# Kernel optimization log

Hardware: AMD Instinct MI355X
Metric: run time of the kernel (lower is better)

Reference implementation:

```python
import jax, jax.numpy as jnp
import numpy as np
from jax import lax

# ---- static graph layout: GPT-2-small-like full edge-pruning config ----
N_LAYERS, H = 12, 12
V_TOTAL = 2 + N_LAYERS * (H + 1)  # wte, wpe, then per layer: H attn outputs + 1 mlp

def _layer_dims(L):
    Vq = 2 + L * (H + 1)  # vertices visible to q/k/v at layer L (strictly upstream)
    Vm = Vq + H           # mlp additionally sees same-layer attn outputs
    return Vq, Vm

_LAYER_BASE = []
_p = 0
for _L in range(N_LAYERS):
    _LAYER_BASE.append(_p)
    _Vq, _Vm = _layer_dims(_L)
    _p += 3 * H * _Vq + _Vm  # q,k,v edges for all heads, then mlp edges
_LM_BASE = _p
P_TOTAL = _p + V_TOTAL       # lm_head reads every vertex


def _keep(Rch):
    """Given per-vertex reachability Rch (bz, V_TOTAL) bool, build the per-edge
    keep mask (bz, P_TOTAL): an edge survives iff its output vertex AND its
    input vertex are both reachable (== ~dangling in the torch code)."""
    bz = Rch.shape[0]
    parts = []
    for L in range(N_LAYERS):
        Vq, Vm = _layer_dims(L)
        a0 = 2 + L * (H + 1)
        ar = Rch[:, a0:a0 + H]        # (bz, H) attn_output-L-h reach
        mr = Rch[:, a0 + H]           # (bz,)  mlp-L reach
        kq = ar[:, None, :, None] & Rch[:, None, None, :Vq]  # (bz,3,H,Vq)
        parts.append(jnp.broadcast_to(kq, (bz, 3, H, Vq)).reshape(bz, 3 * H * Vq))
        parts.append(mr[:, None] & Rch[:, :Vm])
        del kq
    parts.append(Rch)                 # lm_head edges: keep iff input reachable
    return jnp.concatenate(parts, axis=1)


def _prune_dangling_edges(masks):
    bz = masks.shape[0]
    # --- forward reachability (reach-to-input), no-grad boolean sweep ---
    pos = masks > 0.0
    R = jnp.ones((bz, 2), bool)  # wte, wpe always reachable
    for L in range(N_LAYERS):
        Vq, Vm = _layer_dims(L)
        b = _LAYER_BASE[L]
        qkv = pos[:, b:b + 3 * H * Vq].reshape(bz, 3, H, Vq)
        # head reachable iff q AND k AND v each have >=1 live reachable input
        ar = jnp.all(jnp.any(qkv & R[:, None, None, :], axis=-1), axis=1)  # (bz,H)
        R = jnp.concatenate([R, ar], axis=1)                               # size Vm
        mm = pos[:, b + 3 * H * Vq: b + 3 * H * Vq + Vm]
        mr = jnp.any(mm & R, axis=-1)
        R = jnp.concatenate([R, mr[:, None]], axis=1)
    masks = jnp.where(_keep(R), masks, 0.0)
    # --- backward reachability (reach-to-output) on the pruned masks ---
    pos = masks > 0.0
    O = pos[:, _LM_BASE:]  # (bz, V_TOTAL): vertices fed into lm_head
    for L in range(N_LAYERS - 1, -1, -1):
        Vq, Vm = _layer_dims(L)
        b = _LAYER_BASE[L]
        a0 = 2 + L * (H + 1)
        # mlp first (it may make same-layer attn outputs output-reachable)
        mm = pos[:, b + 3 * H * Vq: b + 3 * H * Vq + Vm]
        O = O.at[:, :Vm].set(O[:, :Vm] | (mm & O[:, a0 + H][:, None]))
        qkv = pos[:, b:b + 3 * H * Vq].reshape(bz, 3, H, Vq)
        contrib = jnp.any(qkv & O[:, None, a0:a0 + H, None], axis=(1, 2))  # (bz,Vq)
        O = O.at[:, :Vq].set(O[:, :Vq] | contrib)
    masks = jnp.where(_keep(O), masks, 0.0)
    return masks


def setup_inputs() -> dict:
    key = jax.random.key(0)
    k1, k2 = jax.random.split(key)
    bz = 1024
    sample_params = jax.random.normal(k1, (P_TOTAL,), dtype=jnp.float32)
    unif = jax.random.uniform(k2, (bz, P_TOTAL), dtype=jnp.float32)
    return {"sample_params": sample_params, "unif": unif}


def reference(sample_params, unif):
    bz = unif.shape[0]
    prob = jnp.broadcast_to(jax.nn.sigmoid(sample_params)[None, :], unif.shape)
    window = lax.stop_gradient(prob * (1.0 - prob))  # detached window size
    prob = window * prob + (1.0 - window) * lax.stop_gradient(prob)
    masks = jnp.clip((prob - unif) / window + 0.5, 0.0, 1.0)
    masks = _prune_dangling_edges(masks)
    active = (masks > 0.001) & (masks < 1.0 - 0.001)
    n_samples = jnp.sum(active, axis=0).astype(masks.dtype)  # (P,)
    grad_wts = lax.stop_gradient(
        jnp.where(n_samples < 1.0, 0.0, bz / jnp.maximum(n_samples, 1.0)))
    masks = grad_wts * masks + (1.0 - grad_wts) * lax.stop_gradient(masks)
    return masks
```

## Files before the change

kernel.cpp:

```cpp
#include <hip/hip_runtime.h>
#include <stdint.h>

#define NL   12
#define PTOT 32936
#define LMB  32778
#define NCH  515
#define NCHP 520
#define NGRP 129
#define BMW  (NGRP * 4)
#define TPAD (NGRP * 256)
#define NSEG 445
#define TPB  512
#define NWV  (TPB / 64)
#define NITER ((NGRP + NWV - 1) / NWV)

typedef float vf4 __attribute__((ext_vector_type(4)));

__device__ __constant__ int c_base[NL] = {0,86,653,1701,3230,5240,7731,10703,14156,18090,22505,27401};

__device__ __forceinline__ uint64_t ext(const uint64_t* P, uint32_t off) {
  uint32_t w = off >> 6, s = off & 63;
  uint64_t lo = P[w], hi = P[w + 1];
  return s ? ((lo >> s) | (hi << (64 - s))) : lo;
}

__device__ __forceinline__ uint64_t rbit(uint64_t r0, uint64_t r1, uint64_t r2, uint32_t idx) {
  uint64_t w = idx < 64 ? r0 : (idx < 128 ? r1 : r2);
  return (w >> (idx & 63)) & 1ull;
}

__device__ __forceinline__ uint64_t rext(uint64_t a0, uint64_t a1, uint64_t a2, uint32_t off) {
  uint32_t w = off >> 6, s = off & 63;
  uint64_t lo = (w == 0) ? a0 : ((w == 1) ? a1 : ((w == 2) ? a2 : 0ull));
  uint64_t hi = (w == 0) ? a1 : ((w == 1) ? a2 : 0ull);
  return s ? ((lo >> s) | (hi << (64 - s))) : lo;
}

__device__ __forceinline__ void orAt(uint64_t& r0, uint64_t& r1, uint64_t& r2,
                                     uint64_t val, uint32_t pos) {
  uint32_t w = pos >> 6, s = pos & 63;
  uint64_t lo = val << s;
  uint64_t hi = s ? (val >> (64 - s)) : 0ull;
  if (w == 0) { r0 |= lo; r1 |= hi; }
  else if (w == 1) { r1 |= lo; r2 |= hi; }
  else { r2 |= lo; }
}

__device__ __forceinline__ void maskLen(uint32_t len, uint64_t& m0, uint64_t& m1, uint64_t& m2) {
  m0 = (len >= 64) ? ~0ull : ((1ull << len) - 1ull);
  m1 = (len <= 64) ? 0ull : ((len >= 128) ? ~0ull : ((1ull << (len - 64)) - 1ull));
  m2 = (len <= 128) ? 0ull : ((1ull << (len - 128)) - 1ull);
}

__device__ __forceinline__ uint32_t ext12(uint64_t O0, uint64_t O1, uint64_t O2, uint32_t pos) {
  uint32_t w = pos >> 6, s = pos & 63;
  uint64_t lo = (w == 0) ? O0 : ((w == 1) ? O1 : O2);
  uint64_t hi = (w == 0) ? O1 : ((w == 1) ? O2 : 0ull);
  uint64_t v = s ? ((lo >> s) | (hi << (64 - s))) : lo;
  return (uint32_t)v & 0xFFFu;
}

__device__ __forceinline__ uint64_t spread4(uint64_t x) {
  x = (x | (x << 24)) & 0x000000FF000000FFull;
  x = (x | (x << 12)) & 0x000F000F000F000Full;
  x = (x | (x << 6))  & 0x0303030303030303ull;
  x = (x | (x << 3))  & 0x1111111111111111ull;
  return x;
}

__global__ void init_tables(const float* __restrict__ sp, float* __restrict__ pr,
                            float* __restrict__ wd) {
  int p = blockIdx.x * blockDim.x + threadIdx.x;
  if (p >= TPAD) return;
  if (p < PTOT) {
    float x = sp[p];
    float s = 1.0f / (1.0f + expf(-x));
    float w = __fmul_rn(s, __fsub_rn(1.0f, s));
    float pv = __fadd_rn(__fmul_rn(w, s), __fmul_rn(__fsub_rn(1.0f, w), s));
    pr[p] = pv; wd[p] = w;
  } else {
    pr[p] = 0.0f; wd[p] = 1.0f;
  }
}

__global__ __launch_bounds__(TPB, 4) void fused_kernel(const float* __restrict__ unif,
                                                       const vf4* __restrict__ pr4,
                                                       const vf4* __restrict__ wd4,
                                                       float* __restrict__ out) {
  __shared__ uint64_t sPos[NCHP];
  __shared__ uint64_t sKeep[NCHP];
  __shared__ uint64_t sLv[4];

  const int tid  = threadIdx.x;
  const int lane = tid & 63;
  const int wv   = tid >> 6;
  const int row  = blockIdx.x;
  const vf4* up4 = (const vf4*)(unif + (size_t)row * PTOT);
  vf4*       op4 = (vf4*)(out + (size_t)row * PTOT);

  vf4 mv[NITER];

  {
    vf4 u = {0.f,0.f,0.f,0.f}, p = {0.f,0.f,0.f,0.f}, w = {1.f,1.f,1.f,1.f};
    {
      int e4 = wv * 64 + lane;
      u = up4[e4]; p = pr4[e4]; w = wd4[e4];
    }
#pragma unroll
    for (int k = 0; k < NITER; ++k) {
      const int G = wv + k * NWV;
      const bool act = G < NGRP;
      vf4 un = {0.f,0.f,0.f,0.f}, pn = {0.f,0.f,0.f,0.f}, wn = {1.f,1.f,1.f,1.f};
      if (k + 1 < NITER) {
        const int Gn = G + NWV;
        if (Gn < NGRP) {
          int e4n = Gn * 64 + lane;
          bool inbn = e4n < (PTOT / 4);
          un = inbn ? up4[e4n] : (vf4){0.f,0.f,0.f,0.f};
          pn = pr4[e4n]; wn = wd4[e4n];
        }
      }
      if (act) {
        int e4 = G * 64 + lane;
        bool inb = e4 < (PTOT / 4);
        float m0 = __fadd_rn(__fdiv_rn(__fsub_rn(p.x, u.x), w.x), 0.5f);
        float m1 = __fadd_rn(__fdiv_rn(__fsub_rn(p.y, u.y), w.y), 0.5f);
        float m2 = __fadd_rn(__fdiv_rn(__fsub_rn(p.z, u.z), w.z), 0.5f);
        float m3 = __fadd_rn(__fdiv_rn(__fsub_rn(p.w, u.w), w.w), 0.5f);
        mv[k] = (vf4){m0, m1, m2, m3};
        uint64_t b0 = __ballot(inb && (m0 > 0.0f));
        uint64_t b1 = __ballot(inb && (m1 > 0.0f));
        uint64_t b2 = __ballot(inb && (m2 > 0.0f));
        uint64_t b3 = __ballot(inb && (m3 > 0.0f));
        if (lane < 4) {
          uint64_t v = (lane == 0) ? b0 : (lane == 1) ? b1 : (lane == 2) ? b2 : b3;
          sKeep[G * 4 + lane] = v;
        }
      }
      u = un; p = pn; w = wn;
    }
  }
  __syncthreads();

  for (int G = tid; G < NGRP; G += TPB) {
    uint64_t b0 = sKeep[4 * G], b1 = sKeep[4 * G + 1];
    uint64_t b2 = sKeep[4 * G + 2], b3 = sKeep[4 * G + 3];
#pragma unroll
    for (int q = 0; q < 4; ++q) {
      uint64_t v = spread4((b0 >> (16 * q)) & 0xFFFFull)
                 | (spread4((b1 >> (16 * q)) & 0xFFFFull) << 1)
                 | (spread4((b2 >> (16 * q)) & 0xFFFFull) << 2)
                 | (spread4((b3 >> (16 * q)) & 0xFFFFull) << 3);
      sPos[4 * G + q] = v;
      sKeep[4 * G + q] = 0ull;
    }
  }
  for (int w = BMW + tid; w < NCHP; w += TPB) { sPos[w] = 0ull; sKeep[w] = 0ull; }
  __syncthreads();

  if (tid < 64) {
    uint64_t R0 = 3ull, R1 = 0ull, R2 = 0ull;
    const int g = lane;
#pragma unroll
    for (int L = 0; L < NL; ++L) {
      const int Vq = 2 + 13 * L;
      const int b  = c_base[L];
      bool pred = false;
      if (g < 36) {
        uint32_t off = (uint32_t)(b + g * Vq);
        uint64_t e0 = ext(sPos, off), e1 = ext(sPos, off + 64), e2 = ext(sPos, off + 128);
        pred = ((e0 & R0) | (e1 & R1) | (e2 & R2)) != 0ull;
      }
      uint64_t bal = __ballot(pred);
      uint64_t ar  = bal & (bal >> 12) & (bal >> 24) & 0xFFFull;
      orAt(R0, R1, R2, ar, (uint32_t)Vq);
      const int Vm = Vq + 12;
      uint32_t offm = (uint32_t)(b + 36 * Vq);
      uint64_t e0 = ext(sPos, offm), e1 = ext(sPos, offm + 64), e2 = ext(sPos, offm + 128);
      uint64_t mr = (((e0 & R0) | (e1 & R1) | (e2 & R2)) != 0ull) ? 1ull : 0ull;
      orAt(R0, R1, R2, mr, (uint32_t)Vm);
    }

    uint64_t O0 = ext(sPos, LMB)       & R0;
    uint64_t O1 = ext(sPos, LMB + 64)  & R1;
    uint64_t O2 = ext(sPos, LMB + 128) & ((1ull << 30) - 1ull) & R2;
    const int hg = g % 12;
#pragma unroll
    for (int L = NL - 1; L >= 0; --L) {
      const int Vq = 2 + 13 * L, Vm = Vq + 12;
      const int b  = c_base[L];
      if (rbit(O0, O1, O2, (uint32_t)Vm)) {
        uint64_t m0, m1, m2; maskLen((uint32_t)Vm, m0, m1, m2);
        uint32_t offm = (uint32_t)(b + 36 * Vq);
        O0 |= ext(sPos, offm)       & R0 & m0;
        O1 |= ext(sPos, offm + 64)  & R1 & m1;
        O2 |= ext(sPos, offm + 128) & R2 & m2;
      }
      uint32_t h12 = ext12(O0, O1, O2, (uint32_t)Vq);
      uint64_t q0, q1, q2; maskLen((uint32_t)Vq, q0, q1, q2);
      uint64_t c0 = 0ull, c1 = 0ull, c2 = 0ull;
      if (g < 36 && ((h12 >> hg) & 1u)) {
        uint32_t off = (uint32_t)(b + g * Vq);
        c0 = ext(sPos, off)       & R0 & q0;
        c1 = ext(sPos, off + 64)  & R1 & q1;
        c2 = ext(sPos, off + 128) & R2 & q2;
      }
#pragma unroll
      for (int d = 32; d; d >>= 1) {
        c0 |= __shfl_xor((unsigned long long)c0, d);
        c1 |= __shfl_xor((unsigned long long)c1, d);
        c2 |= __shfl_xor((unsigned long long)c2, d);
      }
      O0 |= c0; O1 |= c1; O2 |= c2;
    }
    if (lane == 0) {
      sLv[0] = R0 & O0; sLv[1] = R1 & O1; sLv[2] = R2 & O2; sLv[3] = 0ull;
    }
  }
  __syncthreads();

  {
    const uint64_t l0 = sLv[0], l1 = sLv[1], l2 = sLv[2];
    for (int s = tid; s < NSEG; s += TPB) {
      uint32_t p0, len;
      bool olive;
      if (s == NSEG - 1) {
        p0 = LMB; len = 158; olive = true;
      } else {
        int L = s / 37, j = s - L * 37;
        int Vq = 2 + 13 * L, b = c_base[L];
        if (j < 36) { p0 = (uint32_t)(b + j * Vq); len = (uint32_t)Vq;
                      olive = rbit(l0, l1, l2, (uint32_t)(Vq + (j % 12))) != 0ull; }
        else        { p0 = (uint32_t)(b + 36 * Vq); len = (uint32_t)(Vq + 12);
                      olive = rbit(l0, l1, l2, (uint32_t)(Vq + 12)) != 0ull; }
      }
      if (!olive) continue;
      uint32_t w0 = p0 >> 6, s0 = p0 & 63;
      uint64_t first = l0;
      if (len < 64) first &= (1ull << len) - 1ull;
      atomicOr((unsigned long long*)&sKeep[w0], (unsigned long long)(first << s0));
      uint32_t done = 64 - s0;
      uint32_t w = w0 + 1;
      while (done < len) {
        uint64_t v = rext(l0, l1, l2, done);
        uint32_t rem = len - done;
        if (rem < 64) v &= (1ull << rem) - 1ull;
        atomicOr((unsigned long long*)&sKeep[w], (unsigned long long)v);
        done += 64; ++w;
      }
    }
  }
  __syncthreads();

  {
    const int sh = 4 * (lane & 15);
    const int kw0 = lane >> 4;
#pragma unroll
    for (int k = 0; k < NITER; ++k) {
      const int G = wv + k * NWV;
      if (G >= NGRP) continue;
      int e4 = G * 64 + lane;
      bool inb = e4 < (PTOT / 4);
      uint32_t kb = (uint32_t)(sKeep[G * 4 + kw0] >> sh) & 0xFu;
      vf4 m = mv[k];
      if (inb) {
        vf4 o;
        o.x = (kb & 1u) ? fminf(fmaxf(m.x, 0.0f), 1.0f) : 0.0f;
        o.y = (kb & 2u) ? fminf(fmaxf(m.y, 0.0f), 1.0f) : 0.0f;
        o.z = (kb & 4u) ? fminf(fmaxf(m.z, 0.0f), 1.0f) : 0.0f;
        o.w = (kb & 8u) ? fminf(fmaxf(m.w, 0.0f), 1.0f) : 0.0f;
        __builtin_nontemporal_store(o, &op4[e4]);
      }
    }
  }
}

extern "C" void kernel_launch(void* const* d_in, const int* in_sizes, int n_in,
                              void* d_out, int out_size, void* d_ws, size_t ws_size,
                              hipStream_t stream) {
  const float* sp   = (const float*)d_in[0];
  const float* unif = (const float*)d_in[1];
  float* out = (float*)d_out;
  char* ws = (char*)d_ws;
  float* pr = (float*)ws;
  float* wd = (float*)(ws + 132096);
  int bz = in_sizes[1] / PTOT;

  init_tables<<<dim3(TPAD / 256), dim3(256), 0, stream>>>(sp, pr, wd);
  fused_kernel<<<dim3(bz), dim3(TPB), 0, stream>>>(
      unif, (const vf4*)pr, (const vf4*)wd, out);
}
```

Baseline: 252.3 us.

## Deepen load prefetch, pack positivity bits in-wave, drop extra sync pass

The load loop now prefetches unif four iterations ahead and prob/window two ahead instead of one. The spread4 bit-interleaving is done directly by lanes 0-3 after the ballots, removing a separate pass over shared memory and one __syncthreads. Clamping moves into the first phase, and launch bounds drop from 4 to 3 blocks per SM to give room for the extra in-flight registers. The aim is more memory-level parallelism and fewer barriers, at the cost of lower occupancy.

```diff
diff --git a/kernel.cpp b/kernel.cpp
--- a/kernel.cpp
+++ b/kernel.cpp
@@ -83,7 +83,7 @@
   }
 }
 
-__global__ __launch_bounds__(TPB, 4) void fused_kernel(const float* __restrict__ unif,
+__global__ __launch_bounds__(TPB, 3) void fused_kernel(const float* __restrict__ unif,
                                                        const vf4* __restrict__ pr4,
                                                        const vf4* __restrict__ wd4,
                                                        float* __restrict__ out) {
@@ -99,63 +99,50 @@
   vf4*       op4 = (vf4*)(out + (size_t)row * PTOT);
 
   vf4 mv[NITER];
-
-  {
-    vf4 u = {0.f,0.f,0.f,0.f}, p = {0.f,0.f,0.f,0.f}, w = {1.f,1.f,1.f,1.f};
-    {
-      int e4 = wv * 64 + lane;
-      u = up4[e4]; p = pr4[e4]; w = wd4[e4];
-    }
-#pragma unroll
-    for (int k = 0; k < NITER; ++k) {
-      const int G = wv + k * NWV;
-      const bool act = G < NGRP;
-      vf4 un = {0.f,0.f,0.f,0.f}, pn = {0.f,0.f,0.f,0.f}, wn = {1.f,1.f,1.f,1.f};
-      if (k + 1 < NITER) {
-        const int Gn = G + NWV;
-        if (Gn < NGRP) {
-          int e4n = Gn * 64 + lane;
-          bool inbn = e4n < (PTOT / 4);
-          un = inbn ? up4[e4n] : (vf4){0.f,0.f,0.f,0.f};
-          pn = pr4[e4n]; wn = wd4[e4n];
-        }
-      }
-      if (act) {
-        int e4 = G * 64 + lane;
-        bool inb = e4 < (PTOT / 4);
-        float m0 = __fadd_rn(__fdiv_rn(__fsub_rn(p.x, u.x), w.x), 0.5f);
-        float m1 = __fadd_rn(__fdiv_rn(__fsub_rn(p.y, u.y), w.y), 0.5f);
-        float m2 = __fadd_rn(__fdiv_rn(__fsub_rn(p.z, u.z), w.z), 0.5f);
-        float m3 = __fadd_rn(__fdiv_rn(__fsub_rn(p.w, u.w), w.w), 0.5f);
-        mv[k] = (vf4){m0, m1, m2, m3};
-        uint64_t b0 = __ballot(inb && (m0 > 0.0f));
-        uint64_t b1 = __ballot(inb && (m1 > 0.0f));
-        uint64_t b2 = __ballot(inb && (m2 > 0.0f));
-        uint64_t b3 = __ballot(inb && (m3 > 0.0f));
-        if (lane < 4) {
-          uint64_t v = (lane == 0) ? b0 : (lane == 1) ? b1 : (lane == 2) ? b2 : b3;
-          sKeep[G * 4 + lane] = v;
-        }
-      }
-      u = un; p = pn; w = wn;
-    }
-  }
-  __syncthreads();
-
-  for (int G = tid; G < NGRP; G += TPB) {
-    uint64_t b0 = sKeep[4 * G], b1 = sKeep[4 * G + 1];
-    uint64_t b2 = sKeep[4 * G + 2], b3 = sKeep[4 * G + 3];
-#pragma unroll
-    for (int q = 0; q < 4; ++q) {
-      uint64_t v = spread4((b0 >> (16 * q)) & 0xFFFFull)
-                 | (spread4((b1 >> (16 * q)) & 0xFFFFull) << 1)
-                 | (spread4((b2 >> (16 * q)) & 0xFFFFull) << 2)
-                 | (spread4((b3 >> (16 * q)) & 0xFFFFull) << 3);
-      sPos[4 * G + q] = v;
-      sKeep[4 * G + q] = 0ull;
-    }
-  }
-  for (int w = BMW + tid; w < NCHP; w += TPB) { sPos[w] = 0ull; sKeep[w] = 0ull; }
+  vf4 ub[4], pb[2], wb[2];
+
+#define LDU(K) do { int G_ = wv + (K) * NWV; if (G_ < NGRP) {                  \
+    int e4_ = G_ * 64 + lane;                                                  \
+    ub[(K) % 4] = (e4_ < (PTOT / 4)) ? up4[e4_] : (vf4){0.f,0.f,0.f,0.f}; } } while (0)
+#define LDPW(K) do { int G_ = wv + (K) * NWV; if (G_ < NGRP) {                 \
+    int e4_ = G_ * 64 + lane;                                                  \
+    pb[(K) % 2] = pr4[e4_]; wb[(K) % 2] = wd4[e4_]; } } while (0)
+
+  LDU(0); LDU(1); LDU(2); LDU(3); LDPW(0); LDPW(1);
+  for (int w = tid; w < NCHP; w += TPB) sKeep[w] = 0ull;
+  for (int w = BMW + tid; w < NCHP; w += TPB) sPos[w] = 0ull;
+
+#pragma unroll
+  for (int k = 0; k < NITER; ++k) {
+    const int G = wv + k * NWV;
+    if (G < NGRP) {
+      vf4 u = ub[k % 4], p = pb[k % 2], w = wb[k % 2];
+      int e4 = G * 64 + lane;
+      bool inb = e4 < (PTOT / 4);
+      float m0 = __fadd_rn(__fdiv_rn(__fsub_rn(p.x, u.x), w.x), 0.5f);
+      float m1 = __fadd_rn(__fdiv_rn(__fsub_rn(p.y, u.y), w.y), 0.5f);
+      float m2 = __fadd_rn(__fdiv_rn(__fsub_rn(p.z, u.z), w.z), 0.5f);
+      float m3 = __fadd_rn(__fdiv_rn(__fsub_rn(p.w, u.w), w.w), 0.5f);
+      mv[k] = (vf4){fminf(fmaxf(m0, 0.0f), 1.0f), fminf(fmaxf(m1, 0.0f), 1.0f),
+                    fminf(fmaxf(m2, 0.0f), 1.0f), fminf(fmaxf(m3, 0.0f), 1.0f)};
+      uint64_t b0 = __ballot(inb && (m0 > 0.0f));
+      uint64_t b1 = __ballot(inb && (m1 > 0.0f));
+      uint64_t b2 = __ballot(inb && (m2 > 0.0f));
+      uint64_t b3 = __ballot(inb && (m3 > 0.0f));
+      if (lane < 4) {
+        int q = lane;
+        uint64_t v = spread4((b0 >> (16 * q)) & 0xFFFFull)
+                   | (spread4((b1 >> (16 * q)) & 0xFFFFull) << 1)
+                   | (spread4((b2 >> (16 * q)) & 0xFFFFull) << 2)
+                   | (spread4((b3 >> (16 * q)) & 0xFFFFull) << 3);
+        sPos[4 * G + q] = v;
+      }
+    }
+    if (k + 4 < NITER) LDU(k + 4);
+    if (k + 2 < NITER) LDPW(k + 2);
+  }
+#undef LDU
+#undef LDPW
   __syncthreads();
 
   if (tid < 64) {
@@ -265,10 +252,10 @@
       vf4 m = mv[k];
       if (inb) {
         vf4 o;
-        o.x = (kb & 1u) ? fminf(fmaxf(m.x, 0.0f), 1.0f) : 0.0f;
-        o.y = (kb & 2u) ? fminf(fmaxf(m.y, 0.0f), 1.0f) : 0.0f;
-        o.z = (kb & 4u) ? fminf(fmaxf(m.z, 0.0f), 1.0f) : 0.0f;
-        o.w = (kb & 8u) ? fminf(fmaxf(m.w, 0.0f), 1.0f) : 0.0f;
+        o.x = (kb & 1u) ? m.x : 0.0f;
+        o.y = (kb & 2u) ? m.y : 0.0f;
+        o.z = (kb & 4u) ? m.z : 0.0f;
+        o.w = (kb & 8u) ? m.w : 0.0f;
         __builtin_nontemporal_store(o, &op4[e4]);
       }
     }
```

Result: no change. 255.1 us (+1.1%).
